# Performance work log

Hardware: AMD Instinct MI355X
Metric: run time of the kernel (lower is better)

The kernel has to match this reference:

```python
import jax, jax.numpy as jnp
import numpy as np

B, T = 32, 512
LATENT, COND, HIDDEN, OUT, E = 64, 448, 1024, 512, 8
INPUT = LATENT + COND            # 512
INTER = LATENT + COND + HIDDEN   # 1536
GATE_H = 64


def setup_inputs() -> dict:
    key = jax.random.key(0)
    ks = jax.random.split(key, 20)
    d = {
        "z": jax.random.normal(ks[0], (B, T, LATENT), dtype=jnp.float32),
        "c": jax.random.normal(ks[1], (B, T, COND), dtype=jnp.float32),
    }
    # expert weights: kaiming-uniform-ish init, biases filled with 0.01 (as in torch code)
    layer_dims = [(INPUT, HIDDEN), (INTER, HIDDEN), (INTER, HIDDEN), (INTER, HIDDEN), (INTER, OUT)]
    for i, (fin, fout) in enumerate(layer_dims):
        bound = float(np.sqrt(6.0 / fin))
        d[f"w{i}"] = jax.random.uniform(ks[2 + i], (E, fin, fout), dtype=jnp.float32, minval=-bound, maxval=bound)
        d[f"b{i}"] = jnp.full((E, fout), 0.01, dtype=jnp.float32)
    # gate MLP: input_size -> 64 -> 64 -> E (stored as [in, out])
    gate_dims = [(INPUT, GATE_H), (GATE_H, GATE_H), (GATE_H, E)]
    for i, (fin, fout) in enumerate(gate_dims):
        bound = float(np.sqrt(1.0 / fin))
        d[f"gw{i}"] = jax.random.uniform(ks[10 + 2 * i], (fin, fout), dtype=jnp.float32, minval=-bound, maxval=bound)
        d[f"gb{i}"] = jax.random.uniform(ks[11 + 2 * i], (fout,), dtype=jnp.float32, minval=-bound, maxval=bound)
    return d


def reference(z, c, w0, b0, w1, b1, w2, b2, w3, b3, w4, b4, gw0, gb0, gw1, gb1, gw2, gb2):
    # gate -> per-token softmax mixing coefficients  [B, T, E]
    x = jnp.concatenate([z, c], axis=-1)
    h = jax.nn.leaky_relu(x @ gw0 + gb0)
    h = jax.nn.leaky_relu(h @ gw1 + gb1)
    coef = jax.nn.softmax(h @ gw2 + gb2, axis=-1)
    # Original computes mixed_weight for every t but baddbmm uses only mixed_weight[:, 0];
    # so the effective per-sequence weight uses coefficients at t=0 only (same math, no huge intermediate).
    coef0 = coef[:, 0]  # [B, E]
    layer_out = c
    layers = [(w0, b0, True), (w1, b1, True), (w2, b2, True), (w3, b3, True), (w4, b4, False)]
    for i, (w, b, act) in enumerate(layers):
        if i == 0:
            inp = jnp.concatenate([z, layer_out], axis=-1)      # [B, T, INPUT]
        else:
            inp = jnp.concatenate([z, c, layer_out], axis=-1)   # [B, T, INTER]
        wm = jnp.einsum('be,eio->bio', coef0, w)                # per-sequence mixed weight
        bm = jnp.einsum('bte,eo->bto', coef, b)                 # per-token mixed bias
        out = bm + jnp.einsum('bti,bio->bto', inp, wm)
        layer_out = jax.nn.leaky_relu(out) if act else out
    return layer_out
```

## Files before the change

### kernel.cpp

```cpp
#include <hip/hip_runtime.h>
#include <math.h>

#define B_     32
#define T_     512
#define LATENT 64
#define COND   448
#define HIDDEN 1024
#define OUTD   512
#define E_     8
#define INPUT_ 512
#define INTER_ 1536
#define GATEH  64
#define NTOK   (B_ * T_)
#define KTAIL  64

typedef __attribute__((ext_vector_type(8))) short short8;
typedef __attribute__((ext_vector_type(4))) float f32x4;

static __device__ __forceinline__ unsigned short f2bf(float x) {
    unsigned u = __float_as_uint(x);
    u += 0x7fffu + ((u >> 16) & 1u);
    return (unsigned short)(u >> 16);
}

__global__ __launch_bounds__(256) void wprep_kernel(
    const float* __restrict__ gw0, const float* __restrict__ gw1,
    unsigned short* __restrict__ gw0T, unsigned short* __restrict__ gw1T)
{
    int idx = blockIdx.x * 256 + threadIdx.x;
    if (idx < GATEH * INPUT_) {
        int n = idx >> 9, k = idx & 511;
        gw0T[n * INPUT_ + k] = f2bf(gw0[k * GATEH + n]);
    } else {
        int i2 = idx - GATEH * INPUT_;
        if (i2 < GATEH * GATEH) {
            int n = i2 >> 6, k = i2 & 63;
            gw1T[n * GATEH + k] = f2bf(gw1[k * GATEH + n]);
        }
    }
}

__global__ __launch_bounds__(256) void gate_kernel(
    const float* __restrict__ z, const float* __restrict__ c,
    const float* __restrict__ gb0,
    const float* __restrict__ gb1,
    const float* __restrict__ gw2, const float* __restrict__ gb2,
    const unsigned short* __restrict__ gw0T,
    const unsigned short* __restrict__ gw1T,
    float* __restrict__ coef, unsigned short* __restrict__ coefpad,
    unsigned short* __restrict__ xzb)
{
    __shared__ unsigned short Hb[GATEH][72];
    __shared__ float H2[GATEH][65];
    __shared__ float sLg[GATEH][E_];

    const int tid = threadIdx.x;
    const int lane = tid & 63;
    const int wv = tid >> 6;
    const int tok0 = blockIdx.x * 64;

#pragma unroll
    for (int i = 0; i < 4; ++i) {
        int idx = i * 256 + tid;
        int tr = idx >> 4, c4 = (idx & 15) * 4;
        float4 v = *(const float4*)(z + ((size_t)(tok0 + tr) * LATENT) + c4);
        ushort4 o = {f2bf(v.x), f2bf(v.y), f2bf(v.z), f2bf(v.w)};
        *(ushort4*)(xzb + (size_t)(tok0 + tr) * INPUT_ + c4) = o;
    }
#pragma unroll
    for (int i = 0; i < 28; ++i) {
        int idx = i * 256 + tid;
        int tr = idx / 112, c4 = (idx % 112) * 4;
        float4 v = *(const float4*)(c + ((size_t)(tok0 + tr) * COND) + c4);
        ushort4 o = {f2bf(v.x), f2bf(v.y), f2bf(v.z), f2bf(v.w)};
        *(ushort4*)(xzb + (size_t)(tok0 + tr) * INPUT_ + LATENT + c4) = o;
    }
    __threadfence_block();
    __syncthreads();

    const int fr = lane & 15, fq = lane >> 4;
    const int wm0 = (wv & 1) * 32, wn0 = (wv >> 1) * 32;

    f32x4 acc[2][2];
#pragma unroll
    for (int im = 0; im < 2; ++im)
#pragma unroll
        for (int in = 0; in < 2; ++in) acc[im][in] = (f32x4){0.f,0.f,0.f,0.f};

    for (int k0 = 0; k0 < INPUT_; k0 += 32) {
        short8 af[2], bf[2];
#pragma unroll
        for (int im = 0; im < 2; ++im)
            af[im] = *(const short8*)(xzb + (size_t)(tok0 + wm0 + im*16 + fr) * INPUT_
                                          + k0 + fq * 8);
#pragma unroll
        for (int in = 0; in < 2; ++in)
            bf[in] = *(const short8*)(gw0T + (size_t)(wn0 + in*16 + fr) * INPUT_
                                           + k0 + fq * 8);
#pragma unroll
        for (int im = 0; im < 2; ++im)
#pragma unroll
            for (int in = 0; in < 2; ++in)
                acc[im][in] = __builtin_amdgcn_mfma_f32_16x16x32_bf16(
                    af[im], bf[in], acc[im][in], 0, 0, 0);
    }
#pragma unroll
    for (int im = 0; im < 2; ++im)
#pragma unroll
        for (int in = 0; in < 2; ++in)
#pragma unroll
            for (int reg = 0; reg < 4; ++reg) {
                int m = wm0 + im*16 + fq*4 + reg;
                int n = wn0 + in*16 + fr;
                float h = acc[im][in][reg] + gb0[n];
                h = h > 0.f ? h : 0.01f * h;
                Hb[m][n] = f2bf(h);
            }
    __syncthreads();

    f32x4 a2[2][2];
#pragma unroll
    for (int im = 0; im < 2; ++im)
#pragma unroll
        for (int in = 0; in < 2; ++in) a2[im][in] = (f32x4){0.f,0.f,0.f,0.f};
#pragma unroll
    for (int k0 = 0; k0 < GATEH; k0 += 32) {
        short8 af[2], bf[2];
#pragma unroll
        for (int im = 0; im < 2; ++im)
            af[im] = *(const short8*)(&Hb[wm0 + im*16 + fr][k0 + fq*8]);
#pragma unroll
        for (int in = 0; in < 2; ++in)
            bf[in] = *(const short8*)(gw1T + (size_t)(wn0 + in*16 + fr) * GATEH
                                           + k0 + fq * 8);
#pragma unroll
        for (int im = 0; im < 2; ++im)
#pragma unroll
            for (int in = 0; in < 2; ++in)
                a2[im][in] = __builtin_amdgcn_mfma_f32_16x16x32_bf16(
                    af[im], bf[in], a2[im][in], 0, 0, 0);
    }
#pragma unroll
    for (int im = 0; im < 2; ++im)
#pragma unroll
        for (int in = 0; in < 2; ++in)
#pragma unroll
            for (int reg = 0; reg < 4; ++reg) {
                int m = wm0 + im*16 + fq*4 + reg;
                int n = wn0 + in*16 + fr;
                float h = a2[im][in][reg] + gb1[n];
                H2[m][n] = h > 0.f ? h : 0.01f * h;
            }
    __syncthreads();

    {
        int tok = tid >> 2, e0 = (tid & 3) * 2;
        float l0 = gb2[e0], l1 = gb2[e0 + 1];
#pragma unroll
        for (int i = 0; i < GATEH; ++i) {
            float h = H2[tok][i];
            l0 = fmaf(h, gw2[i * E_ + e0], l0);
            l1 = fmaf(h, gw2[i * E_ + e0 + 1], l1);
        }
        sLg[tok][e0] = l0; sLg[tok][e0 + 1] = l1;
    }
    __syncthreads();

    if (tid < 64) {
        int token = tok0 + tid;
        float lg[E_], m = -1e30f, s = 0.f;
#pragma unroll
        for (int e = 0; e < E_; ++e) { lg[e] = sLg[tid][e]; m = fmaxf(m, lg[e]); }
#pragma unroll
        for (int e = 0; e < E_; ++e) { lg[e] = expf(lg[e] - m); s += lg[e]; }
        float inv = 1.f / s;
        unsigned short pad[KTAIL];
#pragma unroll
        for (int e = 0; e < E_; ++e) {
            float cv = lg[e] * inv;
            coef[(size_t)token * E_ + e] = cv;
            pad[e] = f2bf(cv);
        }
#pragma unroll
        for (int j = E_; j < KTAIL; ++j) pad[j] = 0;
#pragma unroll
        for (int q = 0; q < KTAIL / 4; ++q)
            *(ushort4*)(coefpad + (size_t)token * KTAIL + q * 4) =
                *(const ushort4*)&pad[q * 4];
    }
}

#define MI 32
#define MO 64
#define MP 65

__global__ __launch_bounds__(256) void mixT_kernel(
    const float* __restrict__ w,
    const float* __restrict__ bias,
    const float* __restrict__ coef,
    unsigned short* __restrict__ wmT,
    int fin, int fout, int gb, int batch0)
{
    __shared__ float sW[E_][MI][MP];
    __shared__ float sC[B_][E_];
    const int t = threadIdx.x;
    const int fin_tot = fin + KTAIL;
    const int nbi = fin / MI;
    const int i0 = (blockIdx.x % nbi) * MI;
    const int o0 = (blockIdx.x / nbi) * MO;

    if (t < gb * E_)
        sC[t >> 3][t & 7] = coef[(size_t)(batch0 + (t >> 3)) * T_ * E_ + (t & 7)];

#pragma unroll
    for (int r = 0; r < 64; ++r) {
        int idx = r * 256 + t;
        int o = idx & 63;
        int i = (idx >> 6) & 31;
        int e = idx >> 11;
        sW[e][i][o] = w[(size_t)e * fin * fout + (size_t)(i0 + i) * fout + o0 + o];
    }
    __syncthreads();

    const int o  = t >> 2;
    const int i8 = (t & 3) * 8;
    for (int b = 0; b < gb; ++b) {
        float v[8];
#pragma unroll
        for (int j = 0; j < 8; ++j) v[j] = 0.f;
#pragma unroll
        for (int e = 0; e < E_; ++e) {
            float cc = sC[b][e];
#pragma unroll
            for (int j = 0; j < 8; ++j)
                v[j] = fmaf(cc, sW[e][i8 + j][o], v[j]);
        }
        unsigned short u[8];
#pragma unroll
        for (int j = 0; j < 8; ++j) u[j] = f2bf(v[j]);
        *(int4*)(wmT + ((size_t)b * fout + o0 + o) * fin_tot + i0 + i8) = *(const int4*)u;
    }

    if (i0 == 0) {
        const int jj = t & 3;
        unsigned short u[8];
#pragma unroll
        for (int q = 0; q < 8; ++q)
            u[q] = (jj == 0) ? f2bf(bias[(size_t)q * fout + o0 + o]) : 0;
        unsigned short z8[8] = {0, 0, 0, 0, 0, 0, 0, 0};
        for (int b = 0; b < gb; ++b) {
            size_t rb = ((size_t)b * fout + o0 + o) * fin_tot + fin;
            *(int4*)(wmT + rb + jj * 8)      = *(const int4*)u;
            *(int4*)(wmT + rb + 32 + jj * 8) = *(const int4*)z8;
        }
    }
}

__global__ __launch_bounds__(512, 2) void gemm_kernel(
    const unsigned short* __restrict__ xz,
    const unsigned short* __restrict__ prev,
    const unsigned short* __restrict__ wmT,
    const unsigned short* __restrict__ coefpad,
    float* __restrict__ outf,
    unsigned short* __restrict__ outb,
    int fin_tot, int fout, int act, int batch0)
{
    __shared__ __align__(16) unsigned short As[2][2][8192];
    __shared__ __align__(16) unsigned short Bs[2][2][8192];

    const int tid = threadIdx.x;
    const int lane = tid & 63;
    const int w8 = tid >> 6;
    const int wm = w8 & 1;
    const int wn = w8 >> 1;

    const int nx = gridDim.x;
    int bx = blockIdx.x, by = blockIdx.y, bz = blockIdx.z;
    {
        int nwg = nx * 2 * gridDim.z;
        if ((nwg & 7) == 0) {
            int f = blockIdx.x + nx * (blockIdx.y + 2 * blockIdx.z);
            int q = nwg >> 3;
            int wk = (f & 7) * q + (f >> 3);
            int bpb = nx * 2;
            bz = wk / bpb;
            int r = wk - bz * bpb;
            by = r / nx;
            bx = r - by * nx;
        }
    }

    const int row0 = by * 256;
    const int col0 = bx * 256;
    const size_t tokbase = (size_t)(batch0 + bz) * T_;
    const unsigned short* wmb = wmT + (size_t)bz * fin_tot * fout;

    const int lrow = lane >> 2;
    const int lk8  = (((lane & 3) ^ ((lane >> 3) & 3)) * 8);
    const int fr = lane & 15, fq = lane >> 4;
    const int koff = (fq ^ ((fr >> 1) & 3)) * 8;
    const int ktail0 = fin_tot - KTAIL;
    const int nt = fin_tot >> 6;

    f32x4 acc[8][4];
#pragma unroll
    for (int im = 0; im < 8; ++im)
#pragma unroll
        for (int in = 0; in < 4; ++in)
            acc[im][in] = (f32x4){0.f, 0.f, 0.f, 0.f};

    auto stageA = [&](int t, int kk) {
        int k32 = (t << 6) + (kk << 5);
        const unsigned short* abase; int astr, acol;
        if (k32 < INPUT_)      { abase = xz;      astr = INPUT_; acol = k32; }
        else if (k32 < ktail0) { abase = prev;    astr = HIDDEN; acol = k32 - INPUT_; }
        else                   { abase = coefpad; astr = KTAIL;  acol = k32 - ktail0; }
        unsigned short* Ab = &As[t & 1][kk][0];
#pragma unroll
        for (int j = 0; j < 2; ++j) {
            int ch = w8 + 8 * j;
            const unsigned short* src = abase
                + (tokbase + row0 + ch * 16 + lrow) * (size_t)astr + acol + lk8;
            __builtin_amdgcn_global_load_lds(
                (const __attribute__((address_space(1))) unsigned int*)(const void*)src,
                (__attribute__((address_space(3))) unsigned int*)(void*)(Ab + ch * 512),
                16, 0, 0);
        }
    };
    auto stageB = [&](int t, int kk) {
        int k32 = (t << 6) + (kk << 5);
        unsigned short* Bb = &Bs[t & 1][kk][0];
#pragma unroll
        for (int j = 0; j < 2; ++j) {
            int ch = w8 + 8 * j;
            const unsigned short* src = wmb
                + (size_t)(col0 + ch * 16 + lrow) * fin_tot + k32 + lk8;
            __builtin_amdgcn_global_load_lds(
                (const __attribute__((address_space(1))) unsigned int*)(const void*)src,
                (__attribute__((address_space(3))) unsigned int*)(void*)(Bb + ch * 512),
                16, 0, 0);
        }
    };

    auto readA4 = [&](const unsigned short* Ak, int im0, short8* af) {
#pragma unroll
        for (int q = 0; q < 4; ++q)
            af[q] = *(const short8*)(Ak + (im0 + q) * 512 + fr * 32 + koff);
    };
    auto readB4 = [&](const unsigned short* Bk, short8* bv) {
#pragma unroll
        for (int q = 0; q < 4; ++q)
            bv[q] = *(const short8*)(Bk + q * 512 + fr * 32 + koff);
    };
    auto mfma16 = [&](int im0, short8* af, short8* bv) {
#pragma unroll
        for (int q = 0; q < 4; ++q)
#pragma unroll
            for (int in = 0; in < 4; ++in)
                acc[im0 + q][in] = __builtin_amdgcn_mfma_f32_16x16x32_bf16(
                    af[q], bv[in], acc[im0 + q][in], 0, 0, 0);
    };

    stageA(0, 0); stageB(0, 0); stageA(0, 1); stageB(0, 1);
    asm volatile("s_waitcnt vmcnt(4)" ::: "memory");
    __builtin_amdgcn_s_barrier();

    for (int t = 0; t < nt - 1; ++t) {
        const int cur = t & 1;
        const unsigned short* A0  = &As[cur][0][wm * 4096];
        const unsigned short* A1  = &As[cur][1][wm * 4096];
        const unsigned short* Bk0 = &Bs[cur][0][wn * 2048];
        const unsigned short* Bk1 = &Bs[cur][1][wn * 2048];
        short8 af[4], bv[4];

        readA4(A0, 0, af); readB4(Bk0, bv);
        stageA(t + 1, 0);
        __builtin_amdgcn_s_barrier();
        asm volatile("s_waitcnt lgkmcnt(0)" ::: "memory");
        __builtin_amdgcn_s_setprio(1);
        mfma16(0, af, bv);
        __builtin_amdgcn_s_setprio(0);
        __builtin_amdgcn_s_barrier();

        readA4(A0, 4, af);
        stageB(t + 1, 0);
        asm volatile("s_waitcnt vmcnt(4)" ::: "memory");
        __builtin_amdgcn_s_barrier();
        asm volatile("s_waitcnt lgkmcnt(0)" ::: "memory");
        __builtin_amdgcn_s_setprio(1);
        mfma16(4, af, bv);
        __builtin_amdgcn_s_setprio(0);
        __builtin_amdgcn_s_barrier();

        readA4(A1, 0, af); readB4(Bk1, bv);
        stageA(t + 1, 1);
        __builtin_amdgcn_s_barrier();
        asm volatile("s_waitcnt lgkmcnt(0)" ::: "memory");
        __builtin_amdgcn_s_setprio(1);
        mfma16(0, af, bv);
        __builtin_amdgcn_s_setprio(0);
        __builtin_amdgcn_s_barrier();

        readA4(A1, 4, af);
        stageB(t + 1, 1);
        asm volatile("s_waitcnt vmcnt(4)" ::: "memory");
        __builtin_amdgcn_s_barrier();
        asm volatile("s_waitcnt lgkmcnt(0)" ::: "memory");
        __builtin_amdgcn_s_setprio(1);
        mfma16(4, af, bv);
        __builtin_amdgcn_s_setprio(0);
        __builtin_amdgcn_s_barrier();
    }

    {
        const int cur = (nt - 1) & 1;
        const unsigned short* A0  = &As[cur][0][wm * 4096];
        const unsigned short* A1  = &As[cur][1][wm * 4096];
        const unsigned short* Bk0 = &Bs[cur][0][wn * 2048];
        const unsigned short* Bk1 = &Bs[cur][1][wn * 2048];
        short8 af[4], bv[4];

        readA4(A0, 0, af); readB4(Bk0, bv);
        __builtin_amdgcn_s_barrier();
        asm volatile("s_waitcnt lgkmcnt(0)" ::: "memory");
        __builtin_amdgcn_s_setprio(1);
        mfma16(0, af, bv);
        __builtin_amdgcn_s_setprio(0);
        __builtin_amdgcn_s_barrier();

        readA4(A0, 4, af);
        asm volatile("s_waitcnt vmcnt(0)" ::: "memory");
        __builtin_amdgcn_s_barrier();
        asm volatile("s_waitcnt lgkmcnt(0)" ::: "memory");
        __builtin_amdgcn_s_setprio(1);
        mfma16(4, af, bv);
        __builtin_amdgcn_s_setprio(0);
        __builtin_amdgcn_s_barrier();

        readA4(A1, 0, af); readB4(Bk1, bv);
        asm volatile("s_waitcnt lgkmcnt(0)" ::: "memory");
        __builtin_amdgcn_s_setprio(1);
        mfma16(0, af, bv);
        __builtin_amdgcn_s_setprio(0);

        readA4(A1, 4, af);
        asm volatile("s_waitcnt lgkmcnt(0)" ::: "memory");
        __builtin_amdgcn_s_setprio(1);
        mfma16(4, af, bv);
        __builtin_amdgcn_s_setprio(0);
    }

#pragma unroll
    for (int im = 0; im < 8; ++im) {
#pragma unroll
        for (int in = 0; in < 4; ++in) {
#pragma unroll
            for (int reg = 0; reg < 4; ++reg) {
                int r = wm * 128 + im * 16 + fq * 4 + reg;
                int col = wn * 64 + in * 16 + fr;
                float v = acc[im][in][reg];
                if (act) v = v > 0.f ? v : 0.01f * v;
                size_t off = (tokbase + row0 + r) * fout + col0 + col;
                if (outb) outb[off] = f2bf(v);
                else      outf[off] = v;
            }
        }
    }
}

extern "C" void kernel_launch(void* const* d_in, const int* in_sizes, int n_in,
                              void* d_out, int out_size, void* d_ws, size_t ws_size,
                              hipStream_t stream)
{
    const float* z = (const float*)d_in[0];
    const float* c = (const float*)d_in[1];
    const float* w[5]  = {(const float*)d_in[2], (const float*)d_in[4],
                          (const float*)d_in[6], (const float*)d_in[8],
                          (const float*)d_in[10]};
    const float* bs[5] = {(const float*)d_in[3], (const float*)d_in[5],
                          (const float*)d_in[7], (const float*)d_in[9],
                          (const float*)d_in[11]};
    const float* gw0 = (const float*)d_in[12]; const float* gb0 = (const float*)d_in[13];
    const float* gw1 = (const float*)d_in[14]; const float* gb1 = (const float*)d_in[15];
    const float* gw2 = (const float*)d_in[16]; const float* gb2 = (const float*)d_in[17];

    const size_t g0t_b  = (size_t)GATEH * INPUT_ * 2;
    const size_t g1t_b  = (size_t)GATEH * GATEH * 2;
    const size_t xz_b   = (size_t)NTOK * INPUT_ * 2;
    const size_t coef_b = (size_t)NTOK * E_ * 4;
    const size_t cpad_b = (size_t)NTOK * KTAIL * 2;
    const size_t act_b  = (size_t)NTOK * HIDDEN * 2;
    const size_t wmun   = (size_t)(INTER_ + KTAIL) * HIDDEN * 2;

    char* p = (char*)d_ws;
    unsigned short* gw0T  = (unsigned short*)p;  p += g0t_b;
    unsigned short* gw1T  = (unsigned short*)p;  p += g1t_b;
    unsigned short* xzb   = (unsigned short*)p;  p += xz_b;
    float*          coef  = (float*)p;           p += coef_b;
    unsigned short* cpad  = (unsigned short*)p;  p += cpad_b;
    unsigned short* actB  = (unsigned short*)p;  p += act_b;

    size_t base = g0t_b + g1t_b + xz_b + coef_b + cpad_b + act_b;
    size_t avail = (ws_size > base) ? ws_size - base : 0;

    int gb;
    unsigned short* actA;
    unsigned short* wmT;
    if (avail >= act_b + 32 * wmun) {
        gb = 32; actA = (unsigned short*)p; p += act_b; wmT = (unsigned short*)p;
    } else {
        actA = (unsigned short*)d_out;
        wmT  = (unsigned short*)p;
        gb = 1;
        for (int g = 16; g >= 2; g >>= 1)
            if (avail >= (size_t)g * wmun) { gb = g; break; }
    }

    wprep_kernel<<<(GATEH * (INPUT_ + GATEH) + 255) / 256, 256, 0, stream>>>(
        gw0, gw1, gw0T, gw1T);
    gate_kernel<<<NTOK / 64, 256, 0, stream>>>(
        z, c, gb0, gb1, gw2, gb2, gw0T, gw1T, coef, cpad, xzb);

    struct L { int fin, fout, act; const unsigned short* in; unsigned short* outb; };
    L Ls[5] = {
        {INPUT_, HIDDEN, 1, actB , actA},
        {INTER_, HIDDEN, 1, actA, actB},
        {INTER_, HIDDEN, 1, actB, actA},
        {INTER_, HIDDEN, 1, actA, actB},
        {INTER_, OUTD,   0, actB, 0},
    };

    for (int Li = 0; Li < 5; ++Li) {
        int fin = Ls[Li].fin, fout = Ls[Li].fout;
        int nblk = (fin / MI) * (fout / MO);
        for (int g = 0; g < B_; g += gb) {
            mixT_kernel<<<nblk, 256, 0, stream>>>(
                w[Li], bs[Li], coef, wmT, fin, fout, gb, g);
            gemm_kernel<<<dim3(fout / 256, T_ / 256, gb), 512, 0, stream>>>(
                xzb, Ls[Li].in, wmT, cpad,
                (float*)d_out, Ls[Li].outb, fin + KTAIL, fout, Ls[Li].act, g);
        }
    }
}
```

Measured before the change: 685.1 us.

## Double-buffer MFMA fragments to overlap LDS reads with compute; vectorize weight mixing

The GEMM main loop now keeps two sets of A/B register fragments, so each quarter-step's LDS reads are issued before the previous quarter's MFMAs. Partial lgkmcnt waits, with sched_barrier fences to stop the compiler reordering, let the MFMAs start while the newer reads are still in flight. Separately, the mixed-weight kernel loads weights as float4 and caches its per-thread weights in registers across batches. The change targets LDS-latency stalls in front of MFMA, at the cost of more vector registers and hand-tuned wait counts that must match the exact instruction order.

Measured after the change: 658.1 us. -3.9%, faster.

```diff
diff --git a/kernel.cpp b/kernel.cpp
--- a/kernel.cpp
+++ b/kernel.cpp
@@ -213,17 +213,27 @@
         sC[t >> 3][t & 7] = coef[(size_t)(batch0 + (t >> 3)) * T_ * E_ + (t & 7)];
 
 #pragma unroll
-    for (int r = 0; r < 64; ++r) {
+    for (int r = 0; r < 16; ++r) {
         int idx = r * 256 + t;
-        int o = idx & 63;
-        int i = (idx >> 6) & 31;
-        int e = idx >> 11;
-        sW[e][i][o] = w[(size_t)e * fin * fout + (size_t)(i0 + i) * fout + o0 + o];
+        int o4 = idx & 15;
+        int i  = (idx >> 4) & 31;
+        int e  = idx >> 9;
+        float4 v = *(const float4*)(w + (size_t)e * fin * fout
+                                      + (size_t)(i0 + i) * fout + o0 + o4 * 4);
+        *(float4*)&sW[e][i][o4 * 4] = v;
     }
     __syncthreads();
 
     const int o  = t >> 2;
     const int i8 = (t & 3) * 8;
+
+    float rw[E_][8];
+#pragma unroll
+    for (int e = 0; e < E_; ++e)
+#pragma unroll
+        for (int j = 0; j < 8; ++j)
+            rw[e][j] = sW[e][i8 + j][o];
+
     for (int b = 0; b < gb; ++b) {
         float v[8];
 #pragma unroll
@@ -233,7 +243,7 @@
             float cc = sC[b][e];
 #pragma unroll
             for (int j = 0; j < 8; ++j)
-                v[j] = fmaf(cc, sW[e][i8 + j][o], v[j]);
+                v[j] = fmaf(cc, rw[e][j], v[j]);
         }
         unsigned short u[8];
 #pragma unroll
@@ -299,6 +309,7 @@
     const int lk8  = (((lane & 3) ^ ((lane >> 3) & 3)) * 8);
     const int fr = lane & 15, fq = lane >> 4;
     const int koff = (fq ^ ((fr >> 1) & 3)) * 8;
+    const int roff = fr * 32 + koff;
     const int ktail0 = fin_tot - KTAIL;
     const int nt = fin_tot >> 6;
 
@@ -342,15 +353,15 @@
         }
     };
 
-    auto readA4 = [&](const unsigned short* Ak, int im0, short8* af) {
+    auto readA = [&](const unsigned short* Ak, int im0, short8* d4) {
 #pragma unroll
         for (int q = 0; q < 4; ++q)
-            af[q] = *(const short8*)(Ak + (im0 + q) * 512 + fr * 32 + koff);
+            d4[q] = *(const short8*)(Ak + (im0 + q) * 512 + roff);
     };
-    auto readB4 = [&](const unsigned short* Bk, short8* bv) {
+    auto readB = [&](const unsigned short* Bk, short8* d4) {
 #pragma unroll
         for (int q = 0; q < 4; ++q)
-            bv[q] = *(const short8*)(Bk + q * 512 + fr * 32 + koff);
+            d4[q] = *(const short8*)(Bk + q * 512 + roff);
     };
     auto mfma16 = [&](int im0, short8* af, short8* bv) {
 #pragma unroll
@@ -361,53 +372,67 @@
                     af[q], bv[in], acc[im0 + q][in], 0, 0, 0);
     };
 
+    short8 afX[4], afY[4], bvA[4], bvB[4];
+
     stageA(0, 0); stageB(0, 0); stageA(0, 1); stageB(0, 1);
-    asm volatile("s_waitcnt vmcnt(4)" ::: "memory");
+    asm volatile("s_waitcnt vmcnt(4)");
     __builtin_amdgcn_s_barrier();
+    readA(&As[0][0][wm * 4096], 0, afX);
+    readB(&Bs[0][0][wn * 2048], bvA);
 
     for (int t = 0; t < nt - 1; ++t) {
-        const int cur = t & 1;
+        const int cur = t & 1, nxt = cur ^ 1;
         const unsigned short* A0  = &As[cur][0][wm * 4096];
         const unsigned short* A1  = &As[cur][1][wm * 4096];
-        const unsigned short* Bk0 = &Bs[cur][0][wn * 2048];
-        const unsigned short* Bk1 = &Bs[cur][1][wn * 2048];
-        short8 af[4], bv[4];
-
-        readA4(A0, 0, af); readB4(Bk0, bv);
+        const unsigned short* B1p = &Bs[cur][1][wn * 2048];
+        const unsigned short* A0n = &As[nxt][0][wm * 4096];
+        const unsigned short* B0n = &Bs[nxt][0][wn * 2048];
+
         stageA(t + 1, 0);
-        __builtin_amdgcn_s_barrier();
-        asm volatile("s_waitcnt lgkmcnt(0)" ::: "memory");
-        __builtin_amdgcn_s_setprio(1);
-        mfma16(0, af, bv);
-        __builtin_amdgcn_s_setprio(0);
-        __builtin_amdgcn_s_barrier();
-
-        readA4(A0, 4, af);
+        readA(A0, 4, afY);
+        __builtin_amdgcn_s_barrier();
+        __builtin_amdgcn_sched_barrier(0);
+        asm volatile("s_waitcnt lgkmcnt(4)");
+        __builtin_amdgcn_sched_barrier(0);
+        __builtin_amdgcn_s_setprio(1);
+        mfma16(0, afX, bvA);
+        __builtin_amdgcn_s_setprio(0);
+        __builtin_amdgcn_s_barrier();
+
         stageB(t + 1, 0);
-        asm volatile("s_waitcnt vmcnt(4)" ::: "memory");
-        __builtin_amdgcn_s_barrier();
-        asm volatile("s_waitcnt lgkmcnt(0)" ::: "memory");
-        __builtin_amdgcn_s_setprio(1);
-        mfma16(4, af, bv);
-        __builtin_amdgcn_s_setprio(0);
-        __builtin_amdgcn_s_barrier();
-
-        readA4(A1, 0, af); readB4(Bk1, bv);
+        asm volatile("s_waitcnt vmcnt(4)");
+        __builtin_amdgcn_s_barrier();
+        readA(A1, 0, afX);
+        readB(B1p, bvB);
+        __builtin_amdgcn_sched_barrier(0);
+        asm volatile("s_waitcnt lgkmcnt(8)");
+        __builtin_amdgcn_sched_barrier(0);
+        __builtin_amdgcn_s_setprio(1);
+        mfma16(4, afY, bvA);
+        __builtin_amdgcn_s_setprio(0);
+        __builtin_amdgcn_s_barrier();
+
         stageA(t + 1, 1);
-        __builtin_amdgcn_s_barrier();
-        asm volatile("s_waitcnt lgkmcnt(0)" ::: "memory");
-        __builtin_amdgcn_s_setprio(1);
-        mfma16(0, af, bv);
-        __builtin_amdgcn_s_setprio(0);
-        __builtin_amdgcn_s_barrier();
-
-        readA4(A1, 4, af);
+        readA(A1, 4, afY);
+        __builtin_amdgcn_s_barrier();
+        __builtin_amdgcn_sched_barrier(0);
+        asm volatile("s_waitcnt lgkmcnt(4)");
+        __builtin_amdgcn_sched_barrier(0);
+        __builtin_amdgcn_s_setprio(1);
+        mfma16(0, afX, bvB);
+        __builtin_amdgcn_s_setprio(0);
+        __builtin_amdgcn_s_barrier();
+
         stageB(t + 1, 1);
-        asm volatile("s_waitcnt vmcnt(4)" ::: "memory");
-        __builtin_amdgcn_s_barrier();
-        asm volatile("s_waitcnt lgkmcnt(0)" ::: "memory");
-        __builtin_amdgcn_s_setprio(1);
-        mfma16(4, af, bv);
+        asm volatile("s_waitcnt vmcnt(4)");
+        __builtin_amdgcn_s_barrier();
+        readA(A0n, 0, afX);
+        readB(B0n, bvA);
+        __builtin_amdgcn_sched_barrier(0);
+        asm volatile("s_waitcnt lgkmcnt(8)");
+        __builtin_amdgcn_sched_barrier(0);
+        __builtin_amdgcn_s_setprio(1);
+        mfma16(4, afY, bvB);
         __builtin_amdgcn_s_setprio(0);
         __builtin_amdgcn_s_barrier();
     }
@@ -416,37 +441,41 @@
         const int cur = (nt - 1) & 1;
         const unsigned short* A0  = &As[cur][0][wm * 4096];
         const unsigned short* A1  = &As[cur][1][wm * 4096];
-        const unsigned short* Bk0 = &Bs[cur][0][wn * 2048];
-        const unsigned short* Bk1 = &Bs[cur][1][wn * 2048];
-        short8 af[4], bv[4];
-
-        readA4(A0, 0, af); readB4(Bk0, bv);
-        __builtin_amdgcn_s_barrier();
-        asm volatile("s_waitcnt lgkmcnt(0)" ::: "memory");
-        __builtin_amdgcn_s_setprio(1);
-        mfma16(0, af, bv);
-        __builtin_amdgcn_s_setprio(0);
-        __builtin_amdgcn_s_barrier();
-
-        readA4(A0, 4, af);
-        asm volatile("s_waitcnt vmcnt(0)" ::: "memory");
-        __builtin_amdgcn_s_barrier();
-        asm volatile("s_waitcnt lgkmcnt(0)" ::: "memory");
-        __builtin_amdgcn_s_setprio(1);
-        mfma16(4, af, bv);
-        __builtin_amdgcn_s_setprio(0);
-        __builtin_amdgcn_s_barrier();
-
-        readA4(A1, 0, af); readB4(Bk1, bv);
-        asm volatile("s_waitcnt lgkmcnt(0)" ::: "memory");
-        __builtin_amdgcn_s_setprio(1);
-        mfma16(0, af, bv);
-        __builtin_amdgcn_s_setprio(0);
-
-        readA4(A1, 4, af);
-        asm volatile("s_waitcnt lgkmcnt(0)" ::: "memory");
-        __builtin_amdgcn_s_setprio(1);
-        mfma16(4, af, bv);
+        const unsigned short* B1p = &Bs[cur][1][wn * 2048];
+
+        readA(A0, 4, afY);
+        __builtin_amdgcn_sched_barrier(0);
+        asm volatile("s_waitcnt lgkmcnt(4)");
+        __builtin_amdgcn_sched_barrier(0);
+        __builtin_amdgcn_s_setprio(1);
+        mfma16(0, afX, bvA);
+        __builtin_amdgcn_s_setprio(0);
+
+        asm volatile("s_waitcnt vmcnt(0)");
+        __builtin_amdgcn_s_barrier();
+
+        readA(A1, 0, afX);
+        readB(B1p, bvB);
+        __builtin_amdgcn_sched_barrier(0);
+        asm volatile("s_waitcnt lgkmcnt(8)");
+        __builtin_amdgcn_sched_barrier(0);
+        __builtin_amdgcn_s_setprio(1);
+        mfma16(4, afY, bvA);
+        __builtin_amdgcn_s_setprio(0);
+
+        readA(A1, 4, afY);
+        __builtin_amdgcn_sched_barrier(0);
+        asm volatile("s_waitcnt lgkmcnt(4)");
+        __builtin_amdgcn_sched_barrier(0);
+        __builtin_amdgcn_s_setprio(1);
+        mfma16(0, afX, bvB);
+        __builtin_amdgcn_s_setprio(0);
+
+        __builtin_amdgcn_sched_barrier(0);
+        asm volatile("s_waitcnt lgkmcnt(0)");
+        __builtin_amdgcn_sched_barrier(0);
+        __builtin_amdgcn_s_setprio(1);
+        mfma16(4, afY, bvB);
         __builtin_amdgcn_s_setprio(0);
     }
 
```
